# Kernel tuning notes

Hardware: AMD Instinct MI355X
Metric: run time of the kernel (lower is better)

## Reference

```python
import jax, jax.numpy as jnp
import numpy as np

N_NODES = 100000


def _gcn_norm(edge_index, n):
    # add self-loops, then symmetric deg^{-1/2} normalization (PyG GCNConv default)
    loop = jnp.arange(n, dtype=edge_index.dtype)
    src = jnp.concatenate([edge_index[0], loop])
    dst = jnp.concatenate([edge_index[1], loop])
    ones = jnp.ones(src.shape[0], dtype=jnp.float32)
    deg = jax.ops.segment_sum(ones, dst, num_segments=n)
    dinv = jnp.where(deg > 0, jax.lax.rsqrt(deg), 0.0)
    norm = dinv[src] * dinv[dst]  # [E + N]
    return src, dst, norm


def _gcn_conv(x, src, dst, norm, W, b, n):
    h = x @ W                                    # [N, out] transform first (out <= in)
    msg = norm[:, None] * h[src]                 # [E+N, out]
    agg = jax.ops.segment_sum(msg, dst, num_segments=n)
    return agg + b


def reference(x, edge_index, W1, b1, W2, b2):
    n = x.shape[0]
    src, dst, norm = _gcn_norm(edge_index, n)
    h = jax.nn.relu(_gcn_conv(x, src, dst, norm, W1, b1, n))
    # dropout is identity in eval mode (training=False)
    h = jax.nn.relu(_gcn_conv(h, src, dst, norm, W2, b2, n))
    return jax.nn.log_softmax(h, axis=1)


def setup_inputs() -> dict:
    key = jax.random.key(0)
    k1, k2, k3, k4 = jax.random.split(key, 4)
    n, e, f, h, c = N_NODES, 1600000, 500, 64, 40
    x = jax.random.normal(k1, (n, f), dtype=jnp.float32)
    edge_index = jax.random.randint(k2, (2, e), 0, n, dtype=jnp.int64)
    W1 = jax.random.normal(k3, (f, h), dtype=jnp.float32) * (1.0 / np.sqrt(f))
    b1 = jnp.zeros((h,), dtype=jnp.float32)
    W2 = jax.random.normal(k4, (h, c), dtype=jnp.float32) * (1.0 / np.sqrt(h))
    b2 = jnp.zeros((c,), dtype=jnp.float32)
    return {"x": x, "edge_index": edge_index, "W1": W1, "b1": b1, "W2": W2, "b2": b2}
```

## Files before the change

### kernel.cpp

```cpp
#include <hip/hip_runtime.h>

#define NN_F 500
#define HID 64
#define NC 40
#define SCAN_T 256
#define SCAN_E 8
#define SCAN_B (SCAN_T * SCAN_E)
#define LDS_S 40

typedef short s8v __attribute__((ext_vector_type(8)));
typedef short s4v __attribute__((ext_vector_type(4)));
typedef float f4v __attribute__((ext_vector_type(4)));

__device__ __forceinline__ unsigned short rne_bf16(float x) {
    unsigned u = __float_as_uint(x);
    return (unsigned short)((u + 0x7fffu + ((u >> 16) & 1u)) >> 16);
}
__device__ __forceinline__ float bf16_lo(unsigned v) {
    return __uint_as_float(v << 16);
}
__device__ __forceinline__ float bf16_hi(unsigned v) {
    return __uint_as_float(v & 0xffff0000u);
}

__device__ __forceinline__ int load_edge(const void* ei, long long idx, int is64) {
    if (is64) return (int)((const long long*)ei)[idx];
    return ((const int*)ei)[idx];
}

__device__ __forceinline__ int detect_is64_block(const void* ei, int E) {
    const unsigned int* w = (const unsigned int*)ei;
    unsigned int acc = 0;
    int i = threadIdx.x;
    if (i < 256 && i < E) acc = w[2 * i + 1];
    int any = __any(acc != 0u);
    __shared__ int red[4];
    if ((threadIdx.x & 63) == 0) red[threadIdx.x >> 6] = any;
    __syncthreads();
    return (red[0] | red[1] | red[2] | red[3]) == 0;
}

__global__ __launch_bounds__(256) void deg_wprep(const void* ei, int* __restrict__ deg,
                                                 const float* __restrict__ W1,
                                                 const float* __restrict__ W2,
                                                 unsigned short* __restrict__ Wt1,
                                                 unsigned short* __restrict__ Wt2,
                                                 int E, int degBlocks) {
    if ((int)blockIdx.x >= degBlocks) {
        int id = ((int)blockIdx.x - degBlocks) * 256 + threadIdx.x;
        if (id < 64 * 512) {
            int nn = id >> 9, k = id & 511;
            Wt1[id] = rne_bf16(k < NN_F ? W1[k * HID + nn] : 0.f);
        } else {
            int id2 = id - 64 * 512;
            if (id2 < 64 * 64) {
                int nn = id2 >> 6, k = id2 & 63;
                Wt2[id2] = rne_bf16(nn < NC ? W2[k * NC + nn] : 0.f);
            }
        }
        return;
    }
    int is64 = detect_is64_block(ei, E);
    long long e = (long long)blockIdx.x * 256 + threadIdx.x;
    if (e < E) {
        int d = load_edge(ei, (long long)E + e, is64);
        atomicAdd(&deg[d], 1);
    }
}

__global__ __launch_bounds__(SCAN_T) void scan1(const int* __restrict__ deg,
                                                int* __restrict__ off,
                                                int* __restrict__ bsums,
                                                float* __restrict__ dinv, int n) {
    __shared__ int lds[SCAN_T];
    int base = blockIdx.x * SCAN_B + threadIdx.x * SCAN_E;
    int v[SCAN_E];
    int local = 0;
#pragma unroll
    for (int k = 0; k < SCAN_E; ++k) {
        int i = base + k;
        v[k] = (i < n) ? deg[i] : 0;
        if (i < n) dinv[i] = rsqrtf((float)v[k] + 1.0f);
        local += v[k];
    }
    lds[threadIdx.x] = local;
    __syncthreads();
    for (int o = 1; o < SCAN_T; o <<= 1) {
        int t = (threadIdx.x >= o) ? lds[threadIdx.x - o] : 0;
        __syncthreads();
        lds[threadIdx.x] += t;
        __syncthreads();
    }
    int prefix = lds[threadIdx.x] - local;
    if (threadIdx.x == SCAN_T - 1) bsums[blockIdx.x] = lds[threadIdx.x];
    int run = prefix;
#pragma unroll
    for (int k = 0; k < SCAN_E; ++k) {
        if (base + k < n) { off[base + k] = run; run += v[k]; }
    }
}

__global__ __launch_bounds__(SCAN_T) void scan_fin(int* __restrict__ off,
                                                   int* __restrict__ cur,
                                                   const int* __restrict__ bsums,
                                                   int n, int nb) {
    const int lane = threadIdx.x & 63;
    int v = (lane < nb && lane < (int)blockIdx.x) ? bsums[lane] : 0;
#pragma unroll
    for (int o = 1; o < 64; o <<= 1) v += __shfl_xor(v, o);
    const int add = v;
    if ((int)blockIdx.x == nb - 1 && threadIdx.x == 0) off[n] = add + bsums[nb - 1];
    int base = blockIdx.x * SCAN_B + threadIdx.x * SCAN_E;
#pragma unroll
    for (int k = 0; k < SCAN_E; ++k) {
        int i = base + k;
        if (i < n) { int t = off[i] + add; off[i] = t; cur[i] = t; }
    }
}

__global__ void scan2(int* bsums, int* off, int nb, int n) {
    if (threadIdx.x == 0 && blockIdx.x == 0) {
        int run = 0;
        for (int i = 0; i < nb; ++i) { int t = bsums[i]; bsums[i] = run; run += t; }
        off[n] = run;
    }
}
__global__ __launch_bounds__(SCAN_T) void scan3(int* __restrict__ off,
                                                int* __restrict__ cur,
                                                const int* __restrict__ bsums, int n) {
    int base = blockIdx.x * SCAN_B + threadIdx.x * SCAN_E;
    int add = bsums[blockIdx.x];
#pragma unroll
    for (int k = 0; k < SCAN_E; ++k) {
        int i = base + k;
        if (i < n) { int v = off[i] + add; off[i] = v; cur[i] = v; }
    }
}

template<int KPAD, bool ABF16, int OUTW>
__device__ __forceinline__ void gemm_tile(const void* Av,
                                          const unsigned short* __restrict__ Wh,
                                          unsigned short* __restrict__ out,
                                          int n, int K, int bIdx,
                                          unsigned short* Xh, unsigned short* Bh) {
    const int t = threadIdx.x;
    const int row0 = bIdx * 128;
    const int wid = t >> 6, lane = t & 63, q = lane >> 4, nn = lane & 15;

    f4v acc[2][4];
#pragma unroll
    for (int mt = 0; mt < 2; ++mt)
#pragma unroll
        for (int ct = 0; ct < 4; ++ct) acc[mt][ct] = (f4v){0.f, 0.f, 0.f, 0.f};

    for (int k0 = 0; k0 < KPAD; k0 += 32) {
        {
            int bn = t >> 2, kq = t & 3;
            *(s8v*)&Bh[bn * LDS_S + kq * 8] = *(const s8v*)&Wh[bn * KPAD + k0 + kq * 8];
        }
        if (ABF16) {
            const unsigned short* A = (const unsigned short*)Av;
            int kq = t & 3, rbase = t >> 2;
#pragma unroll
            for (int rr = 0; rr < 2; ++rr) {
                int row = rr * 64 + rbase;
                int grow = row0 + row;
                s8v h8 = (s8v){0, 0, 0, 0, 0, 0, 0, 0};
                if (grow < n) h8 = *(const s8v*)&A[(long long)grow * KPAD + k0 + kq * 8];
                *(s8v*)&Xh[row * LDS_S + kq * 8] = h8;
            }
        } else {
            const float* A = (const float*)Av;
            int kq = t & 7, rbase = t >> 3;
#pragma unroll
            for (int rr = 0; rr < 4; ++rr) {
                int row = rr * 32 + rbase;
                int grow = row0 + row;
                int k = k0 + kq * 4;
                float v0 = 0.f, v1 = 0.f, v2 = 0.f, v3 = 0.f;
                if (grow < n) {
                    if (k + 4 <= K) {
                        float4 v = *(const float4*)&A[(long long)grow * K + k];
                        v0 = v.x; v1 = v.y; v2 = v.z; v3 = v.w;
                    } else {
                        if (k + 0 < K) v0 = A[(long long)grow * K + k + 0];
                        if (k + 1 < K) v1 = A[(long long)grow * K + k + 1];
                        if (k + 2 < K) v2 = A[(long long)grow * K + k + 2];
                        if (k + 3 < K) v3 = A[(long long)grow * K + k + 3];
                    }
                }
                s4v h4;
                h4[0] = (short)rne_bf16(v0);
                h4[1] = (short)rne_bf16(v1);
                h4[2] = (short)rne_bf16(v2);
                h4[3] = (short)rne_bf16(v3);
                *(s4v*)&Xh[row * LDS_S + kq * 4] = h4;
            }
        }
        __syncthreads();

        const s8v ah0 = *(const s8v*)&Xh[(wid * 32 + nn) * LDS_S + q * 8];
        const s8v ah1 = *(const s8v*)&Xh[(wid * 32 + 16 + nn) * LDS_S + q * 8];
#pragma unroll
        for (int ct = 0; ct < 4; ++ct) {
            const s8v bh = *(const s8v*)&Bh[(ct * 16 + nn) * LDS_S + q * 8];
            acc[0][ct] = __builtin_amdgcn_mfma_f32_16x16x32_bf16(ah0, bh, acc[0][ct], 0, 0, 0);
            acc[1][ct] = __builtin_amdgcn_mfma_f32_16x16x32_bf16(ah1, bh, acc[1][ct], 0, 0, 0);
        }
        __syncthreads();
    }

#pragma unroll
    for (int mt = 0; mt < 2; ++mt)
#pragma unroll
        for (int ct = 0; ct < 4; ++ct) {
            int col = ct * 16 + nn;
            if (col < OUTW) {
#pragma unroll
                for (int r = 0; r < 4; ++r) {
                    int row = row0 + wid * 32 + mt * 16 + q * 4 + r;
                    if (row < n) out[(long long)row * OUTW + col] = rne_bf16(acc[mt][ct][r]);
                }
            }
        }
}

__global__ __launch_bounds__(256) void build_gemm1(const void* ei,
                                                   const float* __restrict__ dinv,
                                                   int* __restrict__ cur,
                                                   int2* __restrict__ csr, int E,
                                                   int gemmBlocks,
                                                   const float* __restrict__ x,
                                                   const unsigned short* __restrict__ Wt1,
                                                   unsigned short* __restrict__ h1, int n) {
    __shared__ unsigned short Xh[128 * LDS_S];
    __shared__ unsigned short Bh[64 * LDS_S];
    if ((int)blockIdx.x < gemmBlocks) {
        gemm_tile<512, false, 64>(x, Wt1, h1, n, NN_F, blockIdx.x, Xh, Bh);
        return;
    }
    int b = (int)blockIdx.x - gemmBlocks;
    int is64 = detect_is64_block(ei, E);
    long long e = (long long)b * 256 + threadIdx.x;
    if (e >= E) return;
    int s = load_edge(ei, e, is64);
    int d = load_edge(ei, (long long)E + e, is64);
    int pos = atomicAdd(&cur[d], 1);
    csr[pos] = make_int2(s, (int)__float_as_uint(dinv[s] * dinv[d]));
}

__global__ __launch_bounds__(256) void gemm2_kernel(const unsigned short* __restrict__ relu1,
                                                    const unsigned short* __restrict__ Wt2,
                                                    unsigned short* __restrict__ h2, int n) {
    __shared__ unsigned short Xh[128 * LDS_S];
    __shared__ unsigned short Bh[64 * LDS_S];
    gemm_tile<64, true, 40>(relu1, Wt2, h2, n, HID, blockIdx.x, Xh, Bh);
}

#define FMA8(W, H)                                          \
    acc[0] = fmaf(W, bf16_lo((H).x), acc[0]);               \
    acc[1] = fmaf(W, bf16_hi((H).x), acc[1]);               \
    acc[2] = fmaf(W, bf16_lo((H).y), acc[2]);               \
    acc[3] = fmaf(W, bf16_hi((H).y), acc[3]);               \
    acc[4] = fmaf(W, bf16_lo((H).z), acc[4]);               \
    acc[5] = fmaf(W, bf16_hi((H).z), acc[5]);               \
    acc[6] = fmaf(W, bf16_lo((H).w), acc[6]);               \
    acc[7] = fmaf(W, bf16_hi((H).w), acc[7])

__global__ __launch_bounds__(256) void gather_l1(const int2* __restrict__ csr,
                                                 const int* __restrict__ off,
                                                 const unsigned short* __restrict__ h,
                                                 const float* __restrict__ dinv,
                                                 const float* __restrict__ b,
                                                 unsigned short* __restrict__ relu1, int n) {
    const int lane = threadIdx.x & 63;
    const int g = lane >> 3, fl = lane & 7;
    const int node = __builtin_amdgcn_readfirstlane(blockIdx.x * 4 + (threadIdx.x >> 6));
    if (node >= n) return;
    const int start = off[node], end = off[node + 1];
    float acc[8];
#pragma unroll
    for (int k = 0; k < 8; ++k) acc[k] = 0.f;
    int j = start;
    for (; j + 16 <= end; j += 16) {
        int2 ea = csr[j + g];
        int2 eb = csr[j + 8 + g];
        uint4 ha = *(const uint4*)(h + (long long)ea.x * 64 + fl * 8);
        uint4 hb = *(const uint4*)(h + (long long)eb.x * 64 + fl * 8);
        float wa = __uint_as_float((unsigned)ea.y);
        float wb = __uint_as_float((unsigned)eb.y);
        FMA8(wa, ha);
        FMA8(wb, hb);
    }
    for (; j < end; j += 8) {
        int jj = j + g;
        int2 e = csr[jj < end ? jj : end - 1];
        float w = (jj < end) ? __uint_as_float((unsigned)e.y) : 0.f;
        uint4 hv = *(const uint4*)(h + (long long)e.x * 64 + fl * 8);
        FMA8(w, hv);
    }
#pragma unroll
    for (int k = 0; k < 8; ++k) {
        acc[k] += __shfl_xor(acc[k], 8);
        acc[k] += __shfl_xor(acc[k], 16);
        acc[k] += __shfl_xor(acc[k], 32);
    }
    if (g == 0) {
        float dv = dinv[node];
        float w = dv * dv;
        uint4 hn = *(const uint4*)(h + (long long)node * 64 + fl * 8);
        FMA8(w, hn);
        float4 b4a = ((const float4*)b)[fl * 2];
        float4 b4b = ((const float4*)b)[fl * 2 + 1];
        float o[8];
        o[0] = acc[0] + b4a.x; o[1] = acc[1] + b4a.y;
        o[2] = acc[2] + b4a.z; o[3] = acc[3] + b4a.w;
        o[4] = acc[4] + b4b.x; o[5] = acc[5] + b4b.y;
        o[6] = acc[6] + b4b.z; o[7] = acc[7] + b4b.w;
        s8v r;
#pragma unroll
        for (int k = 0; k < 8; ++k)
            r[k] = (short)rne_bf16(o[k] > 0.f ? o[k] : 0.f);
        *(s8v*)&relu1[(long long)node * 64 + fl * 8] = r;
    }
}

__global__ __launch_bounds__(256) void gather_l2(const int2* __restrict__ csr,
                                                 const int* __restrict__ off,
                                                 const unsigned short* __restrict__ h,
                                                 const float* __restrict__ dinv,
                                                 const float* __restrict__ b,
                                                 float* __restrict__ out, int n) {
    const int lane = threadIdx.x & 63;
    const int g = lane >> 3, fl = lane & 7;
    const int node = __builtin_amdgcn_readfirstlane(blockIdx.x * 4 + (threadIdx.x >> 6));
    if (node >= n) return;
    const int start = off[node], end = off[node + 1];
    float acc[8];
#pragma unroll
    for (int k = 0; k < 8; ++k) acc[k] = 0.f;
    int j = start;
    for (; j + 16 <= end; j += 16) {
        int2 ea = csr[j + g];
        int2 eb = csr[j + 8 + g];
        if (fl < 5) {
            uint4 ha = *(const uint4*)(h + (long long)ea.x * 40 + fl * 8);
            uint4 hb = *(const uint4*)(h + (long long)eb.x * 40 + fl * 8);
            float wa = __uint_as_float((unsigned)ea.y);
            float wb = __uint_as_float((unsigned)eb.y);
            FMA8(wa, ha);
            FMA8(wb, hb);
        }
    }
    for (; j < end; j += 8) {
        int jj = j + g;
        int2 e = csr[jj < end ? jj : end - 1];
        if (fl < 5) {
            float w = (jj < end) ? __uint_as_float((unsigned)e.y) : 0.f;
            uint4 hv = *(const uint4*)(h + (long long)e.x * 40 + fl * 8);
            FMA8(w, hv);
        }
    }
#pragma unroll
    for (int k = 0; k < 8; ++k) {
        acc[k] += __shfl_xor(acc[k], 8);
        acc[k] += __shfl_xor(acc[k], 16);
        acc[k] += __shfl_xor(acc[k], 32);
    }
    float v[8];
    float vmax = -1e30f;
    if (fl < 5) {
        float dv = dinv[node];
        float w = dv * dv;
        uint4 hn = *(const uint4*)(h + (long long)node * 40 + fl * 8);
        FMA8(w, hn);
        float4 b4a = ((const float4*)b)[fl * 2];
        float4 b4b = ((const float4*)b)[fl * 2 + 1];
        v[0] = acc[0] + b4a.x; v[1] = acc[1] + b4a.y;
        v[2] = acc[2] + b4a.z; v[3] = acc[3] + b4a.w;
        v[4] = acc[4] + b4b.x; v[5] = acc[5] + b4b.y;
        v[6] = acc[6] + b4b.z; v[7] = acc[7] + b4b.w;
#pragma unroll
        for (int k = 0; k < 8; ++k) {
            v[k] = v[k] > 0.f ? v[k] : 0.f;
            vmax = fmaxf(vmax, v[k]);
        }
    }
#pragma unroll
    for (int o = 1; o < 8; o <<= 1) vmax = fmaxf(vmax, __shfl_xor(vmax, o));
    float ssum = 0.f;
    if (fl < 5) {
#pragma unroll
        for (int k = 0; k < 8; ++k) ssum += expf(v[k] - vmax);
    }
#pragma unroll
    for (int o = 1; o < 8; o <<= 1) ssum += __shfl_xor(ssum, o);
    if (g == 0 && fl < 5) {
        float ls = vmax + logf(ssum);
        float4 o0 = make_float4(v[0] - ls, v[1] - ls, v[2] - ls, v[3] - ls);
        float4 o1 = make_float4(v[4] - ls, v[5] - ls, v[6] - ls, v[7] - ls);
        float4* dst = (float4*)(out + (long long)node * NC + fl * 8);
        dst[0] = o0;
        dst[1] = o1;
    }
}

static inline char* align256(char* p) {
    return (char*)(((uintptr_t)p + 255) & ~(uintptr_t)255);
}

extern "C" void kernel_launch(void* const* d_in, const int* in_sizes, int n_in,
                              void* d_out, int out_size, void* d_ws, size_t ws_size,
                              hipStream_t stream) {
    const float* x  = (const float*)d_in[0];
    const void*  ei = d_in[1];
    const float* W1 = (const float*)d_in[2];
    const float* b1 = (const float*)d_in[3];
    const float* W2 = (const float*)d_in[4];
    const float* b2 = (const float*)d_in[5];
    float* out = (float*)d_out;
    const int n = in_sizes[0] / NN_F;
    const int E = in_sizes[1] / 2;
    const int nScanBlocks = (n + SCAN_B - 1) / SCAN_B;
    const int degBlocks = (E + 255) / 256;
    const int gemmBlocks = (n + 127) / 128;

    char* p = (char*)d_ws;
    int* deg  = (int*)p;                 p = align256(p + (size_t)n * sizeof(int));
    int* off  = (int*)p;                 p = align256(p + (size_t)(n + 1) * sizeof(int));
    int* cur  = (int*)p;                 p = align256(p + (size_t)n * sizeof(int));
    int* bsums = (int*)p;                p = align256(p + 256 * sizeof(int));
    float* dinv = (float*)p;             p = align256(p + (size_t)n * sizeof(float));
    int2* csr = (int2*)p;                p = align256(p + (size_t)E * sizeof(int2));
    unsigned short* Wt1 = (unsigned short*)p; p = align256(p + (size_t)64 * 512 * sizeof(short));
    unsigned short* Wt2 = (unsigned short*)p; p = align256(p + (size_t)64 * 64 * sizeof(short));
    unsigned short* h1 = (unsigned short*)p; p = align256(p + (size_t)n * 64 * sizeof(unsigned short));
    unsigned short* relu1 = (unsigned short*)p; p = align256(p + (size_t)n * 64 * sizeof(unsigned short));
    unsigned short* h2 = h1;

    (void)hipMemsetAsync(deg, 0, (size_t)n * sizeof(int), stream);
    deg_wprep<<<degBlocks + 144, 256, 0, stream>>>(ei, deg, W1, W2, Wt1, Wt2, E, degBlocks);

    scan1<<<nScanBlocks, SCAN_T, 0, stream>>>(deg, off, bsums, dinv, n);
    if (nScanBlocks <= 64) {
        scan_fin<<<nScanBlocks, SCAN_T, 0, stream>>>(off, cur, bsums, n, nScanBlocks);
    } else {
        scan2<<<1, 64, 0, stream>>>(bsums, off, nScanBlocks, n);
        scan3<<<nScanBlocks, SCAN_T, 0, stream>>>(off, cur, bsums, n);
    }

    build_gemm1<<<gemmBlocks + degBlocks, 256, 0, stream>>>(ei, dinv, cur, csr, E,
                                                            gemmBlocks, x, Wt1, h1, n);

    gather_l1<<<(n + 3) / 4, 256, 0, stream>>>(csr, off, h1, dinv, b1, relu1, n);
    gemm2_kernel<<<gemmBlocks, 256, 0, stream>>>(relu1, Wt2, h2, n);
    gather_l2<<<(n + 3) / 4, 256, 0, stream>>>(csr, off, h2, dinv, b2, out, n);
}
```

Before: 549.7 us.

## Load A fragments directly into MFMA registers and keep full weight matrix in LDS

Replaces the LDS-staged GEMM tile with a kernel that stages the whole transposed weight matrix in shared memory once and has each wave load its A rows straight from global memory into MFMA operand registers. This removes the per-k-step LDS writes and two barriers per iteration. The CSR build and GEMM1 are no longer fused into one launch, so they run as separate kernels without overlap. The 64 KB of LDS per block for GEMM1 may limit occupancy, and direct global loads of 32-byte strided row chunks may coalesce less well.

Result: slower. 581.1 us (+5.7%).

```diff
diff --git a/kernel.cpp b/kernel.cpp
--- a/kernel.cpp
+++ b/kernel.cpp
@@ -6,10 +6,8 @@
 #define SCAN_T 256
 #define SCAN_E 8
 #define SCAN_B (SCAN_T * SCAN_E)
-#define LDS_S 40
 
 typedef short s8v __attribute__((ext_vector_type(8)));
-typedef short s4v __attribute__((ext_vector_type(4)));
 typedef float f4v __attribute__((ext_vector_type(4)));
 
 __device__ __forceinline__ unsigned short rne_bf16(float x) {
@@ -137,111 +135,12 @@
     }
 }
 
-template<int KPAD, bool ABF16, int OUTW>
-__device__ __forceinline__ void gemm_tile(const void* Av,
-                                          const unsigned short* __restrict__ Wh,
-                                          unsigned short* __restrict__ out,
-                                          int n, int K, int bIdx,
-                                          unsigned short* Xh, unsigned short* Bh) {
-    const int t = threadIdx.x;
-    const int row0 = bIdx * 128;
-    const int wid = t >> 6, lane = t & 63, q = lane >> 4, nn = lane & 15;
-
-    f4v acc[2][4];
-#pragma unroll
-    for (int mt = 0; mt < 2; ++mt)
-#pragma unroll
-        for (int ct = 0; ct < 4; ++ct) acc[mt][ct] = (f4v){0.f, 0.f, 0.f, 0.f};
-
-    for (int k0 = 0; k0 < KPAD; k0 += 32) {
-        {
-            int bn = t >> 2, kq = t & 3;
-            *(s8v*)&Bh[bn * LDS_S + kq * 8] = *(const s8v*)&Wh[bn * KPAD + k0 + kq * 8];
-        }
-        if (ABF16) {
-            const unsigned short* A = (const unsigned short*)Av;
-            int kq = t & 3, rbase = t >> 2;
-#pragma unroll
-            for (int rr = 0; rr < 2; ++rr) {
-                int row = rr * 64 + rbase;
-                int grow = row0 + row;
-                s8v h8 = (s8v){0, 0, 0, 0, 0, 0, 0, 0};
-                if (grow < n) h8 = *(const s8v*)&A[(long long)grow * KPAD + k0 + kq * 8];
-                *(s8v*)&Xh[row * LDS_S + kq * 8] = h8;
-            }
-        } else {
-            const float* A = (const float*)Av;
-            int kq = t & 7, rbase = t >> 3;
-#pragma unroll
-            for (int rr = 0; rr < 4; ++rr) {
-                int row = rr * 32 + rbase;
-                int grow = row0 + row;
-                int k = k0 + kq * 4;
-                float v0 = 0.f, v1 = 0.f, v2 = 0.f, v3 = 0.f;
-                if (grow < n) {
-                    if (k + 4 <= K) {
-                        float4 v = *(const float4*)&A[(long long)grow * K + k];
-                        v0 = v.x; v1 = v.y; v2 = v.z; v3 = v.w;
-                    } else {
-                        if (k + 0 < K) v0 = A[(long long)grow * K + k + 0];
-                        if (k + 1 < K) v1 = A[(long long)grow * K + k + 1];
-                        if (k + 2 < K) v2 = A[(long long)grow * K + k + 2];
-                        if (k + 3 < K) v3 = A[(long long)grow * K + k + 3];
-                    }
-                }
-                s4v h4;
-                h4[0] = (short)rne_bf16(v0);
-                h4[1] = (short)rne_bf16(v1);
-                h4[2] = (short)rne_bf16(v2);
-                h4[3] = (short)rne_bf16(v3);
-                *(s4v*)&Xh[row * LDS_S + kq * 4] = h4;
-            }
-        }
-        __syncthreads();
-
-        const s8v ah0 = *(const s8v*)&Xh[(wid * 32 + nn) * LDS_S + q * 8];
-        const s8v ah1 = *(const s8v*)&Xh[(wid * 32 + 16 + nn) * LDS_S + q * 8];
-#pragma unroll
-        for (int ct = 0; ct < 4; ++ct) {
-            const s8v bh = *(const s8v*)&Bh[(ct * 16 + nn) * LDS_S + q * 8];
-            acc[0][ct] = __builtin_amdgcn_mfma_f32_16x16x32_bf16(ah0, bh, acc[0][ct], 0, 0, 0);
-            acc[1][ct] = __builtin_amdgcn_mfma_f32_16x16x32_bf16(ah1, bh, acc[1][ct], 0, 0, 0);
-        }
-        __syncthreads();
-    }
-
-#pragma unroll
-    for (int mt = 0; mt < 2; ++mt)
-#pragma unroll
-        for (int ct = 0; ct < 4; ++ct) {
-            int col = ct * 16 + nn;
-            if (col < OUTW) {
-#pragma unroll
-                for (int r = 0; r < 4; ++r) {
-                    int row = row0 + wid * 32 + mt * 16 + q * 4 + r;
-                    if (row < n) out[(long long)row * OUTW + col] = rne_bf16(acc[mt][ct][r]);
-                }
-            }
-        }
-}
-
-__global__ __launch_bounds__(256) void build_gemm1(const void* ei,
-                                                   const float* __restrict__ dinv,
-                                                   int* __restrict__ cur,
-                                                   int2* __restrict__ csr, int E,
-                                                   int gemmBlocks,
-                                                   const float* __restrict__ x,
-                                                   const unsigned short* __restrict__ Wt1,
-                                                   unsigned short* __restrict__ h1, int n) {
-    __shared__ unsigned short Xh[128 * LDS_S];
-    __shared__ unsigned short Bh[64 * LDS_S];
-    if ((int)blockIdx.x < gemmBlocks) {
-        gemm_tile<512, false, 64>(x, Wt1, h1, n, NN_F, blockIdx.x, Xh, Bh);
-        return;
-    }
-    int b = (int)blockIdx.x - gemmBlocks;
+__global__ __launch_bounds__(256) void build_kernel(const void* ei,
+                                                    const float* __restrict__ dinv,
+                                                    int* __restrict__ cur,
+                                                    int2* __restrict__ csr, int E) {
     int is64 = detect_is64_block(ei, E);
-    long long e = (long long)b * 256 + threadIdx.x;
+    long long e = (long long)blockIdx.x * 256 + threadIdx.x;
     if (e >= E) return;
     int s = load_edge(ei, e, is64);
     int d = load_edge(ei, (long long)E + e, is64);
@@ -249,12 +148,86 @@
     csr[pos] = make_int2(s, (int)__float_as_uint(dinv[s] * dinv[d]));
 }
 
-__global__ __launch_bounds__(256) void gemm2_kernel(const unsigned short* __restrict__ relu1,
-                                                    const unsigned short* __restrict__ Wt2,
-                                                    unsigned short* __restrict__ h2, int n) {
-    __shared__ unsigned short Xh[128 * LDS_S];
-    __shared__ unsigned short Bh[64 * LDS_S];
-    gemm_tile<64, true, 40>(relu1, Wt2, h2, n, HID, blockIdx.x, Xh, Bh);
+template<int KPAD, bool ABF16, int OUTW>
+__global__ __launch_bounds__(512, 4) void gemm_direct(const void* Av,
+                                                      const unsigned short* __restrict__ Wh,
+                                                      unsigned short* __restrict__ out,
+                                                      int n, int K) {
+    __shared__ unsigned short Bs[64 * KPAD];
+    for (int d = threadIdx.x; d < 64 * KPAD / 8; d += 512) {
+        int kblk = d >> 6, col = d & 63;
+        *(s8v*)&Bs[d * 8] = *(const s8v*)&Wh[col * KPAD + kblk * 8];
+    }
+    __syncthreads();
+
+    const int t = threadIdx.x;
+    const int wave = t >> 6, lane = t & 63, q = lane >> 4, nn = lane & 15;
+    const int base = blockIdx.x * 256 + wave * 32;
+    const int r0 = base + nn, r1 = base + 16 + nn;
+    const long long lr0 = (r0 < n) ? r0 : (n - 1);
+    const long long lr1 = (r1 < n) ? r1 : (n - 1);
+
+    f4v acc[2][4];
+#pragma unroll
+    for (int mt = 0; mt < 2; ++mt)
+#pragma unroll
+        for (int ct = 0; ct < 4; ++ct) acc[mt][ct] = (f4v){0.f, 0.f, 0.f, 0.f};
+
+#pragma unroll 4
+    for (int k0 = 0; k0 < KPAD; k0 += 32) {
+        const int kk = k0 + q * 8;
+        s8v ah0, ah1;
+        if (ABF16) {
+            const unsigned short* A = (const unsigned short*)Av;
+            ah0 = *(const s8v*)&A[lr0 * KPAD + kk];
+            ah1 = *(const s8v*)&A[lr1 * KPAD + kk];
+        } else {
+            const float* A = (const float*)Av;
+            if (kk + 8 <= K) {
+                float4 a0 = *(const float4*)&A[lr0 * K + kk];
+                float4 a1 = *(const float4*)&A[lr0 * K + kk + 4];
+                float4 c0 = *(const float4*)&A[lr1 * K + kk];
+                float4 c1 = *(const float4*)&A[lr1 * K + kk + 4];
+                ah0[0] = (short)rne_bf16(a0.x); ah0[1] = (short)rne_bf16(a0.y);
+                ah0[2] = (short)rne_bf16(a0.z); ah0[3] = (short)rne_bf16(a0.w);
+                ah0[4] = (short)rne_bf16(a1.x); ah0[5] = (short)rne_bf16(a1.y);
+                ah0[6] = (short)rne_bf16(a1.z); ah0[7] = (short)rne_bf16(a1.w);
+                ah1[0] = (short)rne_bf16(c0.x); ah1[1] = (short)rne_bf16(c0.y);
+                ah1[2] = (short)rne_bf16(c0.z); ah1[3] = (short)rne_bf16(c0.w);
+                ah1[4] = (short)rne_bf16(c1.x); ah1[5] = (short)rne_bf16(c1.y);
+                ah1[6] = (short)rne_bf16(c1.z); ah1[7] = (short)rne_bf16(c1.w);
+            } else {
+#pragma unroll
+                for (int j = 0; j < 8; ++j) {
+                    float v0 = (kk + j < K) ? A[lr0 * K + kk + j] : 0.f;
+                    float v1 = (kk + j < K) ? A[lr1 * K + kk + j] : 0.f;
+                    ah0[j] = (short)rne_bf16(v0);
+                    ah1[j] = (short)rne_bf16(v1);
+                }
+            }
+        }
+        const int bbase = ((kk >> 3) * 64) * 8;
+#pragma unroll
+        for (int ct = 0; ct < 4; ++ct) {
+            const s8v bh = *(const s8v*)&Bs[bbase + (ct * 16 + nn) * 8];
+            acc[0][ct] = __builtin_amdgcn_mfma_f32_16x16x32_bf16(ah0, bh, acc[0][ct], 0, 0, 0);
+            acc[1][ct] = __builtin_amdgcn_mfma_f32_16x16x32_bf16(ah1, bh, acc[1][ct], 0, 0, 0);
+        }
+    }
+
+#pragma unroll
+    for (int mt = 0; mt < 2; ++mt)
+#pragma unroll
+        for (int ct = 0; ct < 4; ++ct) {
+            int col = ct * 16 + nn;
+            if (col < OUTW) {
+#pragma unroll
+                for (int r = 0; r < 4; ++r) {
+                    int row = base + mt * 16 + q * 4 + r;
+                    if (row < n) out[(long long)row * OUTW + col] = rne_bf16(acc[mt][ct][r]);
+                }
+            }
+        }
 }
 
 #define FMA8(W, H)                                          \
@@ -423,7 +396,7 @@
     const int E = in_sizes[1] / 2;
     const int nScanBlocks = (n + SCAN_B - 1) / SCAN_B;
     const int degBlocks = (E + 255) / 256;
-    const int gemmBlocks = (n + 127) / 128;
+    const int gBlocks = (n + 255) / 256;
 
     char* p = (char*)d_ws;
     int* deg  = (int*)p;                 p = align256(p + (size_t)n * sizeof(int));
@@ -448,11 +421,10 @@
         scan2<<<1, 64, 0, stream>>>(bsums, off, nScanBlocks, n);
         scan3<<<nScanBlocks, SCAN_T, 0, stream>>>(off, cur, bsums, n);
     }
-
-    build_gemm1<<<gemmBlocks + degBlocks, 256, 0, stream>>>(ei, dinv, cur, csr, E,
-                                                            gemmBlocks, x, Wt1, h1, n);
-
+    build_kernel<<<degBlocks, 256, 0, stream>>>(ei, dinv, cur, csr, E);
+
+    gemm_direct<512, false, 64><<<gBlocks, 512, 0, stream>>>(x, Wt1, h1, n, NN_F);
     gather_l1<<<(n + 3) / 4, 256, 0, stream>>>(csr, off, h1, dinv, b1, relu1, n);
-    gemm2_kernel<<<gemmBlocks, 256, 0, stream>>>(relu1, Wt2, h2, n);
+    gemm_direct<64, true, 40><<<gBlocks, 512, 0, stream>>>(relu1, Wt2, h2, n, HID);
     gather_l2<<<(n + 3) / 4, 256, 0, stream>>>(csr, off, h2, dinv, b2, out, n);
 }
```
